# Kernel optimization log

Measured on AMD Instinct MI355X. Metric: run time of the kernel, lower is better.

## Reference

```python
import jax, jax.numpy as jnp
import numpy as np

D_MODEL = 2048
N_HEADS = 32
N_KVHEADS = 8
HEAD_DIM = D_MODEL // N_HEADS  # 64
N_GROUPS = N_HEADS // N_KVHEADS  # 4
B, L = 2, 2048


def setup_inputs() -> dict:
    key = jax.random.key(0)
    k1, k2, k3 = jax.random.split(key, 3)
    x = jax.random.normal(k1, (B, L, D_MODEL), dtype=jnp.float32)
    W_qkv = jax.random.normal(k2, (D_MODEL, HEAD_DIM * (N_HEADS + 2 * N_KVHEADS)), dtype=jnp.float32) * 0.02
    W_out = jax.random.normal(k3, (D_MODEL, D_MODEL), dtype=jnp.float32) * 0.02
    # additive causal mask, broadcasts over (b, g, h, l, j)
    neg = jnp.float32(-1e9)
    mask = jnp.where(jnp.tril(jnp.ones((L, L), dtype=bool)), jnp.float32(0.0), neg)
    return {"x": x, "mask": mask, "W_qkv": W_qkv, "W_out": W_out}


def reference(x, mask, W_qkv, W_out):
    b, l, _ = x.shape
    qkv = x @ W_qkv  # (b, l, hd*(H + 2*KVH))
    q, k, v = jnp.split(qkv, [N_HEADS * HEAD_DIM, (N_HEADS + N_KVHEADS) * HEAD_DIM], axis=-1)
    # NOTE: faithful to the original: plain row-major reshapes (no seq/head transpose)
    q = q.reshape(b, N_GROUPS, N_KVHEADS, l, HEAD_DIM)  # (b, g, h, l, d)
    k = k.reshape(b, N_KVHEADS, l, HEAD_DIM)            # (b, h, j, d)
    v = v.reshape(b, N_KVHEADS, l, HEAD_DIM)            # (b, h, j, d)
    scores = jnp.einsum('bghld,bhjd->bghlj', q, k) * (HEAD_DIM ** -0.5)
    scores = scores + mask  # mask broadcasts over leading dims
    attn = jax.nn.softmax(scores, axis=-1)
    out = jnp.einsum('bghlj,bhjd->bghld', attn, v)  # (b, g, h, l, d)
    # rearrange 'b g h l d -> b l (g h d)'
    out = jnp.transpose(out, (0, 3, 1, 2, 4)).reshape(b, l, D_MODEL)
    return out @ W_out
```

## Files before the change

### kernel.cpp

```cpp
#include <hip/hip_runtime.h>
#include <stdint.h>


typedef unsigned short u16;
typedef unsigned int u32;
typedef __attribute__((ext_vector_type(8))) short bf16x8;
typedef __attribute__((ext_vector_type(4))) float f32x4;

__device__ __forceinline__ u16 f2bf(float f) {
  union { float f; uint32_t u; } v; v.f = f;
  uint32_t u = v.u;
  u += 0x7fffu + ((u >> 16) & 1u);
  return (u16)(u >> 16);
}

__device__ __forceinline__ f32x4 mfma16(bf16x8 a, bf16x8 b, f32x4 c) {
  return __builtin_amdgcn_mfma_f32_16x16x32_bf16(a, b, c, 0, 0, 0);
}

__device__ __forceinline__ uint32_t cvt_pk_bf16(float a, float b) {
  uint32_t r;
  asm("v_cvt_pk_bf16_f32 %0, %1, %2" : "=v"(r) : "v"(a), "v"(b));
  return r;
}

__device__ __forceinline__ float exp2fast(float x) {
  return __builtin_amdgcn_exp2f(x);
}

__device__ __forceinline__ void gload16(const u16* g, u16* l) {
  __builtin_amdgcn_global_load_lds((__attribute__((address_space(1))) void*)g,
                                   (__attribute__((address_space(3))) void*)l, 16, 0, 0);
}

__global__ __launch_bounds__(256) void cvt_f32_bf16(const float* __restrict__ in,
                                                    u16* __restrict__ out, int n4) {
  int i = blockIdx.x * blockDim.x + threadIdx.x;
  if (i < n4) {
    float4 v = ((const float4*)in)[i];
    uint2 o;
    o.x = (uint32_t)f2bf(v.x) | ((uint32_t)f2bf(v.y) << 16);
    o.y = (uint32_t)f2bf(v.z) | ((uint32_t)f2bf(v.w) << 16);
    ((uint2*)out)[i] = o;
  }
}

__global__ __launch_bounds__(256) void transpose_cvt(const float* __restrict__ in,
                                                     u16* __restrict__ out, int R, int C) {
  __shared__ float tile[32][33];
  int c0 = blockIdx.x * 32, r0 = blockIdx.y * 32;
  int tx = threadIdx.x, ty = threadIdx.y;
#pragma unroll
  for (int k = 0; k < 32; k += 8)
    tile[ty + k][tx] = in[(size_t)(r0 + ty + k) * C + c0 + tx];
  __syncthreads();
#pragma unroll
  for (int k = 0; k < 32; k += 8)
    out[(size_t)(c0 + ty + k) * R + r0 + tx] = f2bf(tile[tx][ty + k]);
}

template <bool OUTF32>
__global__ __launch_bounds__(256) void gemm_bf16(const u16* __restrict__ A,
                                                 const u16* __restrict__ Bt,
                                                 void* __restrict__ C,
                                                 int M, int N, int K) {
  __shared__ __align__(16) u16 As[2][128 * 32];
  __shared__ __align__(16) u16 Bs[2][128 * 32];
  int tid = threadIdx.x;
  int lane = tid & 63, w = tid >> 6;
  int wm = (w >> 1) * 64, wn = (w & 1) * 64;

  int nwg = gridDim.x * gridDim.y;
  int lin = blockIdx.y * gridDim.x + blockIdx.x;
  int lin2 = (lin & 7) * (nwg >> 3) + (lin >> 3);
  int bxs = lin2 % gridDim.x, bys = lin2 / gridDim.x;
  int bm = bys * 128, bn = bxs * 128;

  int c = lane & 15, g = lane >> 4;

  const int srow = w * 16 + (lane >> 2);
  const int scol = (((lane & 3) ^ ((lane >> 3) & 3))) * 8;
  const u16* aP = A + (size_t)(bm + srow) * K + scol;
  const u16* bP = Bt + (size_t)(bn + srow) * K + scol;
  const size_t rowskip = (size_t)64 * K;

  f32x4 zero = {0.f, 0.f, 0.f, 0.f};
  f32x4 acc[4][4];
#pragma unroll
  for (int mi = 0; mi < 4; mi++)
#pragma unroll
    for (int ni = 0; ni < 4; ni++) acc[mi][ni] = zero;

  auto STAGE = [&](int kt, int buf) {
    u16* aL = &As[buf][(w * 16) * 32];
    u16* bL = &Bs[buf][(w * 16) * 32];
    gload16(aP + kt, aL);
    gload16(aP + kt + rowskip, aL + 64 * 32);
    gload16(bP + kt, bL);
    gload16(bP + kt + rowskip, bL + 64 * 32);
  };

  const int nk = K >> 5;
  STAGE(0, 0);
  __syncthreads();

  const int fq = (g ^ ((c >> 1) & 3)) * 8;

  for (int t = 0; t < nk; ++t) {
    const int cur = t & 1;
    if (t + 1 < nk) STAGE((t + 1) << 5, cur ^ 1);
    bf16x8 af[4], bfr[4];
#pragma unroll
    for (int i = 0; i < 4; i++) af[i] = *(const bf16x8*)&As[cur][(wm + i * 16 + c) * 32 + fq];
#pragma unroll
    for (int i = 0; i < 4; i++) bfr[i] = *(const bf16x8*)&Bs[cur][(wn + i * 16 + c) * 32 + fq];
#pragma unroll
    for (int mi = 0; mi < 4; mi++)
#pragma unroll
      for (int ni = 0; ni < 4; ni++)
        acc[mi][ni] = mfma16(af[mi], bfr[ni], acc[mi][ni]);
    __syncthreads();
  }

#pragma unroll
  for (int mi = 0; mi < 4; mi++)
#pragma unroll
    for (int ni = 0; ni < 4; ni++)
#pragma unroll
      for (int i = 0; i < 4; i++) {
        int row = bm + wm + mi * 16 + g * 4 + i;
        int col = bn + wn + ni * 16 + c;
        float v = acc[mi][ni][i];
        if (OUTF32)
          ((float*)C)[(size_t)row * N + col] = v;
        else
          ((u16*)C)[(size_t)row * N + col] = f2bf(v);
      }
}

__global__ __launch_bounds__(256, 2) void attn_fwd(const u16* __restrict__ qkv,
                                                   u16* __restrict__ attn) {
  __shared__ __align__(16) u16 Ks[2][64][72];
  __shared__ __align__(16) u16 Vs[2][64][72];
  __shared__ __align__(16) u16 Ps[4][32][64];
  const int tid = threadIdx.x;
  const int lane = tid & 63, w = tid >> 6;
  const int c = lane & 15, g = lane >> 4;
  const float C2 = 0.18033688011112042f;

  const int bid = blockIdx.x;
  const int slot = bid >> 3;
  const int head = (bid & 7) * 8 + (slot >> 3);
  const int p = slot & 7;
  const int qtA = p, qtB = 15 - p;
  const int b = head >> 5, gh = head & 31, h = gh & 7;
  const u16* qb = qkv + (size_t)b * 6291456;
  const int qbaseA = qtA * 128 + w * 32;
  const int qbaseB = qtB * 128 + w * 32;

  const u16* qrowA = qb + (size_t)(gh * 64 + qtA * 4 + w) * 3072;
  const u16* qrowB = qb + (size_t)(gh * 64 + qtB * 4 + w) * 3072;
  bf16x8 qfA[2][2], qfB[2][2];
#pragma unroll
  for (int qs = 0; qs < 2; qs++)
#pragma unroll
    for (int kd = 0; kd < 2; kd++) {
      qfA[qs][kd] = *(const bf16x8*)(qrowA + (qs * 16 + c) * 64 + kd * 32 + g * 8);
      qfB[qs][kd] = *(const bf16x8*)(qrowB + (qs * 16 + c) * 64 + kd * 32 + g * 8);
    }

  const f32x4 zero = {0.f, 0.f, 0.f, 0.f};
  f32x4 oA[2][4], oB[2][4];
#pragma unroll
  for (int qs = 0; qs < 2; qs++)
#pragma unroll
    for (int dt = 0; dt < 4; dt++) { oA[qs][dt] = zero; oB[qs][dt] = zero; }
  float sA[2] = {0.f, 0.f};
  float sB[2] = {0.f, 0.f};

  const int kj = tid >> 2, kd16 = (tid & 3) * 16;
  const int vj0 = (tid >> 4) * 4, vd = (tid & 15) * 4;
  const int vsw = (tid & 7) << 3;
  uint4 kreg0, kreg1;
  uint2 vreg[4];

  auto LOAD = [&](int t) {
    int j = t * 64 + kj;
    const u16* kr = qb + (size_t)(h * 256 + (j >> 3)) * 3072 + 2048 + (j & 7) * 64;
    kreg0 = *(const uint4*)(kr + kd16);
    kreg1 = *(const uint4*)(kr + kd16 + 8);
#pragma unroll
    for (int r = 0; r < 4; r++) {
      int jv = t * 64 + vj0 + r;
      const u16* vr = qb + (size_t)(h * 256 + (jv >> 3)) * 3072 + 2560 + (jv & 7) * 64;
      vreg[r] = *(const uint2*)(vr + vd);
    }
  };
  auto EX = [](uint2 v, int e) -> uint32_t {
    uint32_t x = (e < 2) ? v.x : v.y;
    return (e & 1) ? (x >> 16) : (x & 0xffffu);
  };
  auto STORE = [&](int buf) {
    *(uint4*)&Ks[buf][kj][kd16] = kreg0;
    *(uint4*)&Ks[buf][kj][kd16 + 8] = kreg1;
#pragma unroll
    for (int e = 0; e < 4; e++) {
      uint2 wv;
      wv.x = EX(vreg[0], e) | (EX(vreg[1], e) << 16);
      wv.y = EX(vreg[2], e) | (EX(vreg[3], e) << 16);
      *(uint2*)&Vs[buf][vd + e][vj0 ^ vsw] = wv;
    }
  };

  auto computeQ = [&](int t, int qbase, bf16x8 (&qf)[2][2], bf16x8 (&kf)[4][2],
                      f32x4 (&o)[2][4], float (&s_i)[2], int cur) {
    const bool diag = (t * 64 + 63 > qbase);
#pragma unroll
    for (int qs = 0; qs < 2; qs++) {
      f32x4 sc[4];
      __builtin_amdgcn_s_setprio(1);
#pragma unroll
      for (int kvt = 0; kvt < 4; kvt++) {
        f32x4 s = mfma16(kf[kvt][0], qf[qs][0], zero);
        sc[kvt] = mfma16(kf[kvt][1], qf[qs][1], s);
      }
      __builtin_amdgcn_s_setprio(0);
      const int q = qbase + qs * 16 + c;
      if (diag) {
#pragma unroll
        for (int kvt = 0; kvt < 4; kvt++)
#pragma unroll
          for (int i = 0; i < 4; i++)
            if (t * 64 + kvt * 16 + g * 4 + i > q) sc[kvt][i] = -1e30f;
      }
      float rs = 0.f;
#pragma unroll
      for (int kvt = 0; kvt < 4; kvt++)
#pragma unroll
        for (int i = 0; i < 4; i++) {
          float pv = exp2fast(sc[kvt][i] * C2);
          sc[kvt][i] = pv;
          rs += pv;
        }
      rs += __shfl_xor(rs, 16);
      rs += __shfl_xor(rs, 32);
      s_i[qs] += rs;
      const int pr = qs * 16 + c;
      const int sw = (c & 7) << 3;
#pragma unroll
      for (int kvt = 0; kvt < 4; kvt++) {
        uint2 pw;
        pw.x = cvt_pk_bf16(sc[kvt][0], sc[kvt][1]);
        pw.y = cvt_pk_bf16(sc[kvt][2], sc[kvt][3]);
        *(uint2*)&Ps[w][pr][(kvt * 16 + g * 4) ^ sw] = pw;
      }
    }
    __builtin_amdgcn_s_setprio(1);
#pragma unroll
    for (int kt2 = 0; kt2 < 2; kt2++) {
      bf16x8 bv[4];
#pragma unroll
      for (int dt = 0; dt < 4; dt++) {
        const int vr = dt * 16 + c;
        const int sv = ((dt * 4 + (c >> 2)) & 7) << 3;
        bv[dt] = *(const bf16x8*)&Vs[cur][vr][(kt2 * 32 + g * 8) ^ sv];
      }
#pragma unroll
      for (int qs = 0; qs < 2; qs++) {
        const int pr = qs * 16 + c;
        bf16x8 pa = *(const bf16x8*)&Ps[w][pr][(kt2 * 32 + g * 8) ^ ((c & 7) << 3)];
#pragma unroll
        for (int dt = 0; dt < 4; dt++) o[qs][dt] = mfma16(pa, bv[dt], o[qs][dt]);
      }
    }
    __builtin_amdgcn_s_setprio(0);
  };

  const int nt = 2 * qtB + 2;
  const int jtA = (qbaseA + 31) >> 6;
  const int jtB = (qbaseB + 31) >> 6;

  LOAD(0);
  STORE(0);
  __syncthreads();

  for (int t = 0; t < nt; ++t) {
    const int cur = t & 1;
    if (t + 1 < nt) LOAD(t + 1);
    if (t <= jtB) {
      bf16x8 kf[4][2];
#pragma unroll
      for (int kvt = 0; kvt < 4; kvt++)
#pragma unroll
        for (int kd = 0; kd < 2; kd++)
          kf[kvt][kd] = *(const bf16x8*)&Ks[cur][kvt * 16 + c][kd * 32 + g * 8];
      if (t <= jtA) computeQ(t, qbaseA, qfA, kf, oA, sA, cur);
      computeQ(t, qbaseB, qfB, kf, oB, sB, cur);
    }
    if (t + 1 < nt) STORE(cur ^ 1);
    __syncthreads();
  }

  auto epi = [&](int qbase, f32x4 (&o)[2][4], float (&s_i)[2]) {
#pragma unroll
    for (int qs = 0; qs < 2; qs++)
#pragma unroll
      for (int i = 0; i < 4; i++) {
        float sd = __shfl(s_i[qs], g * 4 + i);
        float inv = 1.0f / sd;
        int row = qbase + qs * 16 + g * 4 + i;
        u16* orow = attn + ((size_t)(b * 2048 + row)) * 2048 + gh * 64;
#pragma unroll
        for (int dt = 0; dt < 4; dt++) orow[dt * 16 + c] = f2bf(o[qs][dt][i] * inv);
      }
  };
  epi(qbaseA, oA, sA);
  epi(qbaseB, oB, sB);
}

extern "C" void kernel_launch(void* const* d_in, const int* in_sizes, int n_in,
                              void* d_out, int out_size, void* d_ws, size_t ws_size,
                              hipStream_t stream) {
  const float* x = (const float*)d_in[0];
  const float* Wqkv = (const float*)d_in[2];
  const float* Wout = (const float*)d_in[3];
  float* out = (float*)d_out;

  u16* xb = (u16*)d_ws;
  u16* wqkvT = xb + 8388608;
  u16* woutT = wqkvT + 6291456;
  u16* qkv = woutT + 4194304;
  u16* attn = qkv + 12582912;

  cvt_f32_bf16<<<8192, 256, 0, stream>>>(x, xb, 2097152);
  transpose_cvt<<<dim3(3072 / 32, 2048 / 32), dim3(32, 8), 0, stream>>>(Wqkv, wqkvT, 2048, 3072);
  transpose_cvt<<<dim3(2048 / 32, 2048 / 32), dim3(32, 8), 0, stream>>>(Wout, woutT, 2048, 2048);
  gemm_bf16<false><<<dim3(3072 / 128, 4096 / 128), 256, 0, stream>>>(xb, wqkvT, qkv, 4096, 3072, 2048);
  attn_fwd<<<512, 256, 0, stream>>>(qkv, attn);
  gemm_bf16<true><<<dim3(2048 / 128, 4096 / 128), 256, 0, stream>>>(attn, woutT, out, 4096, 2048, 2048);
}
```

Baseline: 190.2 us.

## Split paired causal q-tiles into one q-tile per block, 1024 blocks

The attention kernel previously gave each block two query tiles (p and 15-p) to balance causal work. It now handles one query tile per block over twice as many blocks, ordered heaviest-first, and raises the launch-bounds occupancy hint from 2 to 3. This halves register state per block and exposes more parallelism, but each K/V tile is now loaded once per q-tile instead of being shared by the pair, and load balance now relies on the hardware scheduler.

```diff
diff --git a/kernel.cpp b/kernel.cpp
--- a/kernel.cpp
+++ b/kernel.cpp
@@ -138,7 +138,7 @@
       }
 }
 
-__global__ __launch_bounds__(256, 2) void attn_fwd(const u16* __restrict__ qkv,
+__global__ __launch_bounds__(256, 3) void attn_fwd(const u16* __restrict__ qkv,
                                                    u16* __restrict__ attn) {
   __shared__ __align__(16) u16 Ks[2][64][72];
   __shared__ __align__(16) u16 Vs[2][64][72];
@@ -150,33 +150,27 @@
 
   const int bid = blockIdx.x;
   const int slot = bid >> 3;
-  const int head = (bid & 7) * 8 + (slot >> 3);
-  const int p = slot & 7;
-  const int qtA = p, qtB = 15 - p;
+  const int head = (bid & 7) * 8 + (slot >> 4);
+  const int qt = 15 - (slot & 15);
   const int b = head >> 5, gh = head & 31, h = gh & 7;
   const u16* qb = qkv + (size_t)b * 6291456;
-  const int qbaseA = qtA * 128 + w * 32;
-  const int qbaseB = qtB * 128 + w * 32;
-
-  const u16* qrowA = qb + (size_t)(gh * 64 + qtA * 4 + w) * 3072;
-  const u16* qrowB = qb + (size_t)(gh * 64 + qtB * 4 + w) * 3072;
-  bf16x8 qfA[2][2], qfB[2][2];
+  const int qbase = qt * 128 + w * 32;
+
+  const u16* qrow = qb + (size_t)(gh * 64 + qt * 4 + w) * 3072;
+  bf16x8 qf[2][2];
 #pragma unroll
   for (int qs = 0; qs < 2; qs++)
 #pragma unroll
-    for (int kd = 0; kd < 2; kd++) {
-      qfA[qs][kd] = *(const bf16x8*)(qrowA + (qs * 16 + c) * 64 + kd * 32 + g * 8);
-      qfB[qs][kd] = *(const bf16x8*)(qrowB + (qs * 16 + c) * 64 + kd * 32 + g * 8);
-    }
+    for (int kd = 0; kd < 2; kd++)
+      qf[qs][kd] = *(const bf16x8*)(qrow + (qs * 16 + c) * 64 + kd * 32 + g * 8);
 
   const f32x4 zero = {0.f, 0.f, 0.f, 0.f};
-  f32x4 oA[2][4], oB[2][4];
+  f32x4 o[2][4];
 #pragma unroll
   for (int qs = 0; qs < 2; qs++)
 #pragma unroll
-    for (int dt = 0; dt < 4; dt++) { oA[qs][dt] = zero; oB[qs][dt] = zero; }
-  float sA[2] = {0.f, 0.f};
-  float sB[2] = {0.f, 0.f};
+    for (int dt = 0; dt < 4; dt++) o[qs][dt] = zero;
+  float s_i[2] = {0.f, 0.f};
 
   const int kj = tid >> 2, kd16 = (tid & 3) * 16;
   const int vj0 = (tid >> 4) * 4, vd = (tid & 15) * 4;
@@ -212,8 +206,7 @@
     }
   };
 
-  auto computeQ = [&](int t, int qbase, bf16x8 (&qf)[2][2], bf16x8 (&kf)[4][2],
-                      f32x4 (&o)[2][4], float (&s_i)[2], int cur) {
+  auto computeQ = [&](int t, bf16x8 (&kf)[4][2], int cur) {
     const bool diag = (t * 64 + 63 > qbase);
 #pragma unroll
     for (int qs = 0; qs < 2; qs++) {
@@ -276,9 +269,8 @@
     __builtin_amdgcn_s_setprio(0);
   };
 
-  const int nt = 2 * qtB + 2;
-  const int jtA = (qbaseA + 31) >> 6;
-  const int jtB = (qbaseB + 31) >> 6;
+  const int nt = 2 * qt + 2;
+  const int jt = (qbase + 31) >> 6;
 
   LOAD(0);
   STORE(0);
@@ -287,35 +279,30 @@
   for (int t = 0; t < nt; ++t) {
     const int cur = t & 1;
     if (t + 1 < nt) LOAD(t + 1);
-    if (t <= jtB) {
+    if (t <= jt) {
       bf16x8 kf[4][2];
 #pragma unroll
       for (int kvt = 0; kvt < 4; kvt++)
 #pragma unroll
         for (int kd = 0; kd < 2; kd++)
           kf[kvt][kd] = *(const bf16x8*)&Ks[cur][kvt * 16 + c][kd * 32 + g * 8];
-      if (t <= jtA) computeQ(t, qbaseA, qfA, kf, oA, sA, cur);
-      computeQ(t, qbaseB, qfB, kf, oB, sB, cur);
+      computeQ(t, kf, cur);
     }
     if (t + 1 < nt) STORE(cur ^ 1);
     __syncthreads();
   }
 
-  auto epi = [&](int qbase, f32x4 (&o)[2][4], float (&s_i)[2]) {
-#pragma unroll
-    for (int qs = 0; qs < 2; qs++)
-#pragma unroll
-      for (int i = 0; i < 4; i++) {
-        float sd = __shfl(s_i[qs], g * 4 + i);
-        float inv = 1.0f / sd;
-        int row = qbase + qs * 16 + g * 4 + i;
-        u16* orow = attn + ((size_t)(b * 2048 + row)) * 2048 + gh * 64;
-#pragma unroll
-        for (int dt = 0; dt < 4; dt++) orow[dt * 16 + c] = f2bf(o[qs][dt][i] * inv);
-      }
-  };
-  epi(qbaseA, oA, sA);
-  epi(qbaseB, oB, sB);
+#pragma unroll
+  for (int qs = 0; qs < 2; qs++)
+#pragma unroll
+    for (int i = 0; i < 4; i++) {
+      float sd = __shfl(s_i[qs], g * 4 + i);
+      float inv = 1.0f / sd;
+      int row = qbase + qs * 16 + g * 4 + i;
+      u16* orow = attn + ((size_t)(b * 2048 + row)) * 2048 + gh * 64;
+#pragma unroll
+      for (int dt = 0; dt < 4; dt++) orow[dt * 16 + c] = f2bf(o[qs][dt][i] * inv);
+    }
 }
 
 extern "C" void kernel_launch(void* const* d_in, const int* in_sizes, int n_in,
@@ -336,6 +323,6 @@
   transpose_cvt<<<dim3(3072 / 32, 2048 / 32), dim3(32, 8), 0, stream>>>(Wqkv, wqkvT, 2048, 3072);
   transpose_cvt<<<dim3(2048 / 32, 2048 / 32), dim3(32, 8), 0, stream>>>(Wout, woutT, 2048, 2048);
   gemm_bf16<false><<<dim3(3072 / 128, 4096 / 128), 256, 0, stream>>>(xb, wqkvT, qkv, 4096, 3072, 2048);
-  attn_fwd<<<512, 256, 0, stream>>>(qkv, attn);
+  attn_fwd<<<1024, 256, 0, stream>>>(qkv, attn);
   gemm_bf16<true><<<dim3(2048 / 128, 4096 / 128), 256, 0, stream>>>(attn, woutT, out, 4096, 2048, 2048);
 }
```

Result: slower. 208.3 us (+9.5%).
